# Performance work log

Hardware: AMD Instinct MI355X
Metric: run time of the kernel (lower is better)

The kernel has to match this reference:

```python
import jax, jax.numpy as jnp
import numpy as np

EPS = 1e-5
LOCAL_WINDOW = 256
NUM_HEADS = 16


def _layernorm(x, g, b):
    m = jnp.mean(x, axis=-1, keepdims=True)
    v = jnp.mean(jnp.square(x - m), axis=-1, keepdims=True)
    return (x - m) * jax.lax.rsqrt(v + EPS) * g + b


def _rotate_half(x):
    x1, x2 = jnp.split(x, 2, axis=-1)
    return jnp.concatenate([-x2, x1], axis=-1)


def _rope_cos_sin(s, d, base=10000.0):
    half = d // 2
    inv_freq = 1.0 / base ** (jnp.arange(half, dtype=jnp.float32) / float(half))
    t = jnp.arange(s, dtype=jnp.float32)
    freqs = jnp.einsum('s,d->sd', t, inv_freq)          # [s, half]
    emb = jnp.concatenate([freqs, freqs], axis=-1)       # [s, d]
    return jnp.cos(emb)[None, None, :, :], jnp.sin(emb)[None, None, :, :]


def setup_inputs() -> dict:
    key = jax.random.key(0)
    ks = jax.random.split(key, 8)
    B, S, D, F = 2, 2048, 1024, 4096
    sc = lambda d: 1.0 / np.sqrt(d)
    return {
        'x': jax.random.normal(ks[0], (B, S, D), jnp.float32),
        'w_qkv': jax.random.normal(ks[1], (D, 3 * D), jnp.float32) * sc(D),
        'w_out': jax.random.normal(ks[2], (D, D), jnp.float32) * sc(D),
        'g1': jnp.ones((D,), jnp.float32),
        'b1': jnp.zeros((D,), jnp.float32),
        'g2': jnp.ones((D,), jnp.float32),
        'b2': jnp.zeros((D,), jnp.float32),
        'w_gate': jax.random.normal(ks[3], (D, F), jnp.float32) * sc(D),
        'b_gate': jnp.zeros((F,), jnp.float32),
        'w_up': jax.random.normal(ks[4], (D, F), jnp.float32) * sc(D),
        'b_up': jnp.zeros((F,), jnp.float32),
        'w_down': jax.random.normal(ks[5], (F, D), jnp.float32) * sc(F),
        'b_down': jnp.zeros((D,), jnp.float32),
    }


def reference(x, w_qkv, w_out, g1, b1, g2, b2, w_gate, b_gate, w_up, b_up, w_down, b_down):
    B, S, D = x.shape
    H = NUM_HEADS
    hd = D // H

    # ---- pre-norm + RoPE self-attention ----
    y = _layernorm(x, g1, b1)
    qkv = jnp.einsum('bsd,de->bse', y, w_qkv)
    q, k, v = jnp.split(qkv, 3, axis=-1)
    split_heads = lambda t: t.reshape(B, S, H, hd).transpose(0, 2, 1, 3)  # [b,h,s,hd]
    q, k, v = split_heads(q), split_heads(k), split_heads(v)

    cos, sin = _rope_cos_sin(S, hd)
    q = q * cos + _rotate_half(q) * sin
    k = k * cos + _rotate_half(k) * sin

    scale = float(hd) ** -0.5
    logits = jnp.einsum('bhid,bhjd->bhij', q, k) * scale

    i = jnp.arange(S)[:, None]
    j = jnp.arange(S)[None, :]
    can = (jnp.abs(j - i) <= LOCAL_WINDOW) & (j <= i)    # local + causal band
    logits = jnp.where(can[None, None], logits, jnp.float32(-1e9))

    attn = jax.nn.softmax(logits, axis=-1)
    o = jnp.einsum('bhij,bhjd->bhid', attn, v)
    o = o.transpose(0, 2, 1, 3).reshape(B, S, D)
    x = x + jnp.einsum('bsd,de->bse', o, w_out)

    # ---- pre-norm + SwiGLU MLP ----
    y = _layernorm(x, g2, b2)
    gate = jnp.einsum('bsd,df->bsf', y, w_gate) + b_gate
    up = jnp.einsum('bsd,df->bsf', y, w_up) + b_up
    gated = gate * jax.nn.silu(up)
    x = x + jnp.einsum('bsf,fd->bsd', gated, w_down) + b_down
    return x
```

## Files before the change

kernel.cpp:

```cpp
#include <hip/hip_runtime.h>

typedef unsigned short u16;
typedef unsigned long long u64;
typedef __attribute__((ext_vector_type(8))) short bf16x8;
typedef __attribute__((ext_vector_type(4))) float f32x4;

__device__ inline u16 f2bf(float f) {
  unsigned int u = __float_as_uint(f);
  u += 0x7fffu + ((u >> 16) & 1u);
  return (u16)(u >> 16);
}
__device__ inline float bf2f(u16 h) { return __uint_as_float(((unsigned int)h) << 16); }

__device__ inline void gload_lds16(const void* gp, void* lp) {
  __builtin_amdgcn_global_load_lds(
      (const __attribute__((address_space(1))) unsigned int*)gp,
      (__attribute__((address_space(3))) unsigned int*)lp, 16, 0, 0);
}

__global__ __launch_bounds__(256) void ln_kernel(const float* __restrict__ x,
                                                 const float* __restrict__ g,
                                                 const float* __restrict__ beta,
                                                 u16* __restrict__ y) {
  __shared__ float red[8];
  const int row = blockIdx.x;
  const int t = threadIdx.x;
  const float4 xv = *(const float4*)(x + (long)row * 1024 + t * 4);
  float s = xv.x + xv.y + xv.z + xv.w;
  float sq = xv.x * xv.x + xv.y * xv.y + xv.z * xv.z + xv.w * xv.w;
#pragma unroll
  for (int d = 1; d < 64; d <<= 1) {
    s += __shfl_xor(s, d);
    sq += __shfl_xor(sq, d);
  }
  if ((t & 63) == 0) { red[t >> 6] = s; red[4 + (t >> 6)] = sq; }
  __syncthreads();
  s = red[0] + red[1] + red[2] + red[3];
  sq = red[4] + red[5] + red[6] + red[7];
  const float mean = s * (1.f / 1024.f);
  const float var = sq * (1.f / 1024.f) - mean * mean;
  const float inv = rsqrtf(var + 1e-5f);
  float xe[4] = {xv.x, xv.y, xv.z, xv.w};
  u16 ov[4];
#pragma unroll
  for (int e = 0; e < 4; ++e)
    ov[e] = f2bf((xe[e] - mean) * inv * g[t * 4 + e] + beta[t * 4 + e]);
  *(u64*)(y + (long)row * 1024 + t * 4) = *(u64*)ov;
}

__global__ __launch_bounds__(256) void transpose_bf16(const float* __restrict__ in,
                                                      u16* __restrict__ out,
                                                      int R, int C) {
  __shared__ float tile[64][33];
  const int t = threadIdx.x;
  const int tx = t & 31, ty = t >> 5;
  const int rx = t & 63, cy = t >> 6;
  const long r0 = (long)blockIdx.y * 64, c0 = (long)blockIdx.x * 32;
#pragma unroll
  for (int i = 0; i < 8; ++i)
    tile[ty + i * 8][tx] = in[(r0 + ty + i * 8) * C + c0 + tx];
  __syncthreads();
#pragma unroll
  for (int i = 0; i < 8; ++i)
    out[(c0 + i * 4 + cy) * R + r0 + rx] = f2bf(tile[rx][i * 4 + cy]);
}

__global__ __launch_bounds__(256) void trig_kernel(float* __restrict__ tbl) {
  const int i = blockIdx.x * 256 + threadIdx.x;
  const int s = i >> 5, d0 = i & 31;
  const float inv = exp2f((float)d0 * (-13.287712379549449f / 32.f));
  float sn, cs;
  sincosf((float)s * inv, &sn, &cs);
  tbl[i] = cs;
  tbl[65536 + i] = sn;
}

__global__ __launch_bounds__(64, 4) void attn_kernel(const u16* __restrict__ qr,
                                                     const u16* __restrict__ kr,
                                                     const u16* __restrict__ vt,
                                                     u16* __restrict__ o) {
  __shared__ __attribute__((aligned(16))) u16 Pl[16][40];
  int wg = blockIdx.x;
  wg = (wg & 7) * 512 + (wg >> 3);
  const int qt = wg & 127;
  const int bh = wg >> 7;
  const int qs = qt * 16;
  const int l = threadIdx.x;
  const int lr = l & 15, lg = l >> 4;
  const long bho = (long)(bh >> 4) * 2048 * 1024 + (long)(bh & 15) * 64;
  const long vtb = (long)bh * 64 * 2048;

  const u16* qp = qr + bho + (long)(qs + lr) * 1024 + lg * 8;
  const bf16x8 aq0 = *(const bf16x8*)qp;
  const bf16x8 aq1 = *(const bf16x8*)(qp + 32);

  f32x4 oacc[4];
#pragma unroll
  for (int nt = 0; nt < 4; ++nt) { oacc[nt][0] = 0.f; oacc[nt][1] = 0.f; oacc[nt][2] = 0.f; oacc[nt][3] = 0.f; }
  float m_[4], ls[4];
#pragma unroll
  for (int r = 0; r < 4; ++r) { m_[r] = -1e30f; ls[r] = 0.f; }

  for (int ch = 0; ch < 9; ++ch) {
    const int j0 = qs - 256 + ch * 32;
    if (j0 + 32 <= 0) continue;

    const int jc0u = j0 + lr;
    const int jc1u = j0 + 16 + lr;
    const int jc0 = min(max(jc0u, 0), 2047);
    const int jc1 = min(max(jc1u, 0), 2047);
    const u16* kp0 = kr + bho + (long)jc0 * 1024 + lg * 8;
    const u16* kp1 = kr + bho + (long)jc1 * 1024 + lg * 8;
    const bf16x8 b00 = *(const bf16x8*)kp0;
    const bf16x8 b01 = *(const bf16x8*)(kp0 + 32);
    const bf16x8 b10 = *(const bf16x8*)kp1;
    const bf16x8 b11 = *(const bf16x8*)(kp1 + 32);

    f32x4 z; z[0] = 0.f; z[1] = 0.f; z[2] = 0.f; z[3] = 0.f;
    f32x4 s0 = __builtin_amdgcn_mfma_f32_16x16x32_bf16(aq0, b00, z, 0, 0, 0);
    s0 = __builtin_amdgcn_mfma_f32_16x16x32_bf16(aq1, b01, s0, 0, 0, 0);
    f32x4 s1 = __builtin_amdgcn_mfma_f32_16x16x32_bf16(aq0, b10, z, 0, 0, 0);
    s1 = __builtin_amdgcn_mfma_f32_16x16x32_bf16(aq1, b11, s1, 0, 0, 0);

    float p0[4], p1[4], al[4];
#pragma unroll
    for (int r = 0; r < 4; ++r) {
      const int qg = qs + lg * 4 + r;
      const bool v0 = (jc0u >= 0) & (jc0u <= qg) & (qg - jc0u <= 256);
      const bool v1 = (jc1u >= 0) & (jc1u <= qg) & (qg - jc1u <= 256);
      const float t0 = v0 ? s0[r] : -1e30f;
      const float t1 = v1 ? s1[r] : -1e30f;
      float mx = fmaxf(t0, t1);
      mx = fmaxf(mx, __shfl_xor(mx, 1));
      mx = fmaxf(mx, __shfl_xor(mx, 2));
      mx = fmaxf(mx, __shfl_xor(mx, 4));
      mx = fmaxf(mx, __shfl_xor(mx, 8));
      const float mn = fmaxf(m_[r], mx);
      if (mn < -1e29f) {
        al[r] = 1.f; p0[r] = 0.f; p1[r] = 0.f;
      } else {
        al[r] = __expf(m_[r] - mn);
        p0[r] = (t0 < -1e29f) ? 0.f : __expf(t0 - mn);
        p1[r] = (t1 < -1e29f) ? 0.f : __expf(t1 - mn);
      }
      m_[r] = mn;
      float rs = p0[r] + p1[r];
      rs += __shfl_xor(rs, 1);
      rs += __shfl_xor(rs, 2);
      rs += __shfl_xor(rs, 4);
      rs += __shfl_xor(rs, 8);
      ls[r] = ls[r] * al[r] + rs;
    }
#pragma unroll
    for (int r = 0; r < 4; ++r) {
      Pl[lg * 4 + r][lr] = f2bf(p0[r]);
      Pl[lg * 4 + r][lr + 16] = f2bf(p1[r]);
    }
    asm volatile("s_waitcnt lgkmcnt(0)" ::: "memory");
    const bf16x8 pa = *(const bf16x8*)(&Pl[lr][lg * 8]);

    const int jb = min(max(j0 + lg * 8, 0), 2040);
    const u16* vp = vt + vtb + (long)lr * 2048 + jb;
#pragma unroll
    for (int nt = 0; nt < 4; ++nt) {
      const bf16x8 bv = *(const bf16x8*)(vp + (long)(nt * 16) * 2048);
      f32x4 oa = oacc[nt];
#pragma unroll
      for (int r = 0; r < 4; ++r) oa[r] *= al[r];
      oacc[nt] = __builtin_amdgcn_mfma_f32_16x16x32_bf16(pa, bv, oa, 0, 0, 0);
    }
  }
#pragma unroll
  for (int nt = 0; nt < 4; ++nt)
#pragma unroll
    for (int r = 0; r < 4; ++r) {
      const long qg = qs + lg * 4 + r;
      o[bho + qg * 1024 + nt * 16 + lr] = f2bf(oacc[nt][r] / ls[r]);
    }
}

__device__ __forceinline__ void stage_half(u16* lds, int ldsbase,
                                           const u16* gp, int ld, int col,
                                           int tid, int w) {
  const int r0 = tid >> 3;
  const int sw = ((tid & 7) ^ (r0 & 7)) << 3;
  gload_lds16(gp + (long)r0 * ld + col + sw, lds + ldsbase + w * 512);
  gload_lds16(gp + (long)(r0 + 64) * ld + col + sw, lds + ldsbase + 4096 + w * 512);
}

template <int EPI>
__global__ __launch_bounds__(512, 2) void gemm8p(const u16* __restrict__ A,
                                                 const u16* __restrict__ BT,
                                                 u16* __restrict__ Cb,
                                                 const float* __restrict__ bias,
                                                 const u16* __restrict__ gate,
                                                 float* __restrict__ Cf0,
                                                 float* __restrict__ Cf1,
                                                 u16* __restrict__ P1,
                                                 u16* __restrict__ P2,
                                                 const float* __restrict__ tbl,
                                                 int M, int N, int Kfull, int Kl) {
  __shared__ __attribute__((aligned(16))) u16 lds[81920];
  const int tid = threadIdx.x;
  const int w = tid >> 6, l = tid & 63;
  const int lr = l & 15, lg = l >> 4;
  const int l7 = l & 7;
  const int wr = w >> 2, wc = w & 3;
  const int nbx = N >> 8, nby = M >> 8;
  int wg = blockIdx.x;
  { const int cpx = gridDim.x >> 3; wg = (wg & 7) * cpx + (wg >> 3); }
  const int z = wg / (nbx * nby);
  const int rem = wg % (nbx * nby);
  const long m0 = (long)(rem / nbx) * 256;
  const long n0 = (long)(rem % nbx) * 256;
  const long koff = (long)z * Kl;
  const int NT = Kl >> 6;

  f32x4 acc[8][4];
#pragma unroll
  for (int i = 0; i < 8; ++i)
#pragma unroll
    for (int j = 0; j < 4; ++j) { acc[i][j][0] = 0.f; acc[i][j][1] = 0.f; acc[i][j][2] = 0.f; acc[i][j][3] = 0.f; }

  const u16* Alo = A + m0 * Kfull + koff;
  const u16* Ahi = A + (m0 + 128) * Kfull + koff;
  const u16* Blo = BT + n0 * Kfull + koff;
  const u16* Bhi = BT + (n0 + 128) * Kfull + koff;

  stage_half(lds, 0, Alo, Kfull, 0, tid, w);
  stage_half(lds, 8192, Ahi, Kfull, 0, tid, w);
  stage_half(lds, 49152, Blo, Kfull, 0, tid, w);
  stage_half(lds, 57344, Bhi, Kfull, 0, tid, w);
  stage_half(lds, 16384, Alo, Kfull, 64, tid, w);
  stage_half(lds, 24576, Ahi, Kfull, 64, tid, w);
  stage_half(lds, 65536, Blo, Kfull, 64, tid, w);
  stage_half(lds, 73728, Bhi, Kfull, 64, tid, w);
  asm volatile("s_waitcnt vmcnt(8)" ::: "memory");
  __builtin_amdgcn_s_barrier();

  for (int t = 0; t < NT; ++t) {
    const int abuf = t % 3;
    int sA = abuf + 2; if (sA >= 3) sA -= 3;
    const int p = t & 1;
    const int baA = abuf * 16384 + wr * 8192;
    const int bB = 49152 + p * 16384;
    bf16x8 b[4][2];
#pragma unroll
    for (int q = 0; q < 4; ++q) {
      bf16x8 a[2][2];
#pragma unroll
      for (int m2 = 0; m2 < 2; ++m2) {
        const int rowA = (q * 2 + m2) * 16 + lr;
#pragma unroll
        for (int kh = 0; kh < 2; ++kh)
          a[m2][kh] = *(const bf16x8*)(lds + baA + rowA * 64 + (((kh * 4 + lg) ^ l7) << 3));
      }
      if (q == 0) {
#pragma unroll
        for (int fn = 0; fn < 4; ++fn) {
          const int rb = wc * 64 + fn * 16 + lr;
#pragma unroll
          for (int kh = 0; kh < 2; ++kh)
            b[fn][kh] = *(const bf16x8*)(lds + bB + (rb >> 7) * 8192 + (rb & 127) * 64 + (((kh * 4 + lg) ^ l7) << 3));
        }
      }
      if (t + 2 < NT) {
        if (q == 0) stage_half(lds, sA * 16384, Alo, Kfull, (t + 2) * 64, tid, w);
        if (q == 1) stage_half(lds, sA * 16384 + 8192, Ahi, Kfull, (t + 2) * 64, tid, w);
        if (q == 2) stage_half(lds, bB, Blo, Kfull, (t + 2) * 64, tid, w);
        if (q == 3) stage_half(lds, bB + 8192, Bhi, Kfull, (t + 2) * 64, tid, w);
      }

      __builtin_amdgcn_s_barrier();
      asm volatile("s_waitcnt lgkmcnt(0)" ::: "memory");
      __builtin_amdgcn_s_setprio(1);
#pragma unroll
      for (int m2 = 0; m2 < 2; ++m2)
#pragma unroll
        for (int fn = 0; fn < 4; ++fn)
#pragma unroll
          for (int kh = 0; kh < 2; ++kh)
            acc[q * 2 + m2][fn] = __builtin_amdgcn_mfma_f32_16x16x32_bf16(a[m2][kh], b[fn][kh], acc[q * 2 + m2][fn], 0, 0, 0);
      __builtin_amdgcn_s_setprio(0);
      if (q == 3) {
        if (t + 2 < NT) { asm volatile("s_waitcnt vmcnt(8)" ::: "memory"); }
        else            { asm volatile("s_waitcnt vmcnt(0)" ::: "memory"); }
      }
      __builtin_amdgcn_s_barrier();
    }
  }

  if constexpr (EPI == 6) {
    const int regn = (int)((n0 + wc * 64) >> 10);
    if (regn < 2) {
      const float scale = (regn == 0) ? 0.125f : 1.f;
      u16* dst = (regn == 0) ? Cb : P1;
      const int cbase = (int)(n0 & 1023) + wc * 64 + lr;
#pragma unroll
      for (int fm = 0; fm < 8; ++fm) {
        const long mr = m0 + wr * 128 + fm * 16 + lg * 4;
#pragma unroll
        for (int fn = 0; fn < 2; ++fn) {
          const int c1 = cbase + fn * 16;
          const int d0 = fn * 16 + lr;
#pragma unroll
          for (int r = 0; r < 4; ++r) {
            const long row = mr + r;
            const int s = (int)(row & 2047);
            const float cs = tbl[(s << 5) + d0];
            const float sn = tbl[65536 + (s << 5) + d0];
            const float x1v = acc[fm][fn][r], x2v = acc[fm][fn + 2][r];
            dst[row * 1024 + c1] = f2bf((x1v * cs - x2v * sn) * scale);
            dst[row * 1024 + c1 + 32] = f2bf((x2v * cs + x1v * sn) * scale);
          }
        }
      }
    } else {
#pragma unroll
      for (int fm = 0; fm < 8; ++fm) {
        const long mr = m0 + wr * 128 + fm * 16 + lg * 4;
        const int bb = (int)(mr >> 11);
        const int s = (int)(mr & 2047);
#pragma unroll
        for (int fn = 0; fn < 4; ++fn) {
          const int ncv = (int)(n0 - 2048) + wc * 64 + fn * 16 + lr;
          const int h = ncv >> 6, d = ncv & 63;
          u16 pk[4];
#pragma unroll
          for (int r = 0; r < 4; ++r) pk[r] = f2bf(acc[fm][fn][r]);
          *(u64*)(P2 + (long)(bb * 16 + h) * 131072 + (long)d * 2048 + s) = *(u64*)pk;
        }
      }
    }
    return;
  }

  float* Cf = nullptr;
  if constexpr (EPI == 0) Cf = (z < 2 ? Cf0 : Cf1) + (long)(z & 1) * M * N;

#pragma unroll
  for (int fm = 0; fm < 8; ++fm) {
    const long mr = m0 + wr * 128 + fm * 16 + lg * 4;
#pragma unroll
    for (int fn = 0; fn < 4; ++fn) {
      const long nc = n0 + wc * 64 + fn * 16 + lr;
#pragma unroll
      for (int r = 0; r < 4; ++r) {
        const long idx = (mr + r) * N + nc;
        const float v = acc[fm][fn][r];
        if constexpr (EPI == 5) {
          Cb[idx] = f2bf(v);
        } else if constexpr (EPI == 2) {
          Cb[idx] = f2bf(v + bias[nc]);
        } else if constexpr (EPI == 3) {
          const float u = v + bias[nc];
          const float sg = 1.f / (1.f + __expf(-u));
          Cb[idx] = f2bf(bf2f(gate[idx]) * u * sg);
        } else if constexpr (EPI == 0) {
          Cf[idx] = v;
        }
      }
    }
  }
}

__global__ __launch_bounds__(256) void combine_ln(const float* __restrict__ p0,
                                                  const float* __restrict__ p1,
                                                  const float* __restrict__ x,
                                                  const float* __restrict__ g,
                                                  const float* __restrict__ beta,
                                                  float* __restrict__ x1,
                                                  u16* __restrict__ y) {
  __shared__ float red[8];
  const long MN = (long)4096 * 1024;
  const int row = blockIdx.x;
  const int t = threadIdx.x;
  const long base = (long)row * 1024 + t * 4;
  const float4 a = *(const float4*)(p0 + base);
  const float4 b = *(const float4*)(p0 + MN + base);
  const float4 c = *(const float4*)(p1 + base);
  const float4 d = *(const float4*)(p1 + MN + base);
  const float4 r = *(const float4*)(x + base);
  float v[4] = {a.x + b.x + c.x + d.x + r.x, a.y + b.y + c.y + d.y + r.y,
                a.z + b.z + c.z + d.z + r.z, a.w + b.w + c.w + d.w + r.w};
  *(float4*)(x1 + base) = *(float4*)v;
  float s = v[0] + v[1] + v[2] + v[3];
  float sq = v[0] * v[0] + v[1] * v[1] + v[2] * v[2] + v[3] * v[3];
#pragma unroll
  for (int dd = 1; dd < 64; dd <<= 1) {
    s += __shfl_xor(s, dd);
    sq += __shfl_xor(sq, dd);
  }
  if ((t & 63) == 0) { red[t >> 6] = s; red[4 + (t >> 6)] = sq; }
  __syncthreads();
  s = red[0] + red[1] + red[2] + red[3];
  sq = red[4] + red[5] + red[6] + red[7];
  const float mean = s * (1.f / 1024.f);
  const float var = sq * (1.f / 1024.f) - mean * mean;
  const float inv = rsqrtf(var + 1e-5f);
  u16 ov[4];
#pragma unroll
  for (int e = 0; e < 4; ++e)
    ov[e] = f2bf((v[e] - mean) * inv * g[t * 4 + e] + beta[t * 4 + e]);
  *(u64*)(y + base) = *(u64*)ov;
}

__global__ __launch_bounds__(256) void combine4(const float* __restrict__ p0,
                                                const float* __restrict__ p1,
                                                const float* __restrict__ res,
                                                const float* __restrict__ bias,
                                                float* __restrict__ out) {
  const long MN = (long)4096 * 1024;
  const long i = ((long)blockIdx.x * 256 + threadIdx.x) * 4;
  const float4 a = *(const float4*)(p0 + i);
  const float4 b = *(const float4*)(p0 + MN + i);
  const float4 c = *(const float4*)(p1 + i);
  const float4 d = *(const float4*)(p1 + MN + i);
  const float4 r = *(const float4*)(res + i);
  const float4 bb = *(const float4*)(bias + (int)(i & 1023));
  float4 o;
  o.x = a.x + b.x + c.x + d.x + r.x + bb.x;
  o.y = a.y + b.y + c.y + d.y + r.y + bb.y;
  o.z = a.z + b.z + c.z + d.z + r.z + bb.z;
  o.w = a.w + b.w + c.w + d.w + r.w + bb.w;
  *(float4*)(out + i) = o;
}

extern "C" void kernel_launch(void* const* d_in, const int* in_sizes, int n_in,
                              void* d_out, int out_size, void* d_ws, size_t ws_size,
                              hipStream_t stream) {
  (void)in_sizes; (void)n_in; (void)out_size; (void)ws_size;
  const float* x      = (const float*)d_in[0];
  const float* w_qkv  = (const float*)d_in[1];
  const float* w_out  = (const float*)d_in[2];
  const float* g1     = (const float*)d_in[3];
  const float* b1     = (const float*)d_in[4];
  const float* g2     = (const float*)d_in[5];
  const float* b2     = (const float*)d_in[6];
  const float* w_gate = (const float*)d_in[7];
  const float* b_gate = (const float*)d_in[8];
  const float* w_up   = (const float*)d_in[9];
  const float* b_up   = (const float*)d_in[10];
  const float* w_down = (const float*)d_in[11];
  const float* b_down = (const float*)d_in[12];
  float* out = (float*)d_out;

  const size_t MB = 1u << 20;
  char* ws = (char*)d_ws;
  u16*   wdownT = (u16*)(ws + 0 * MB);
  u16*   y      = (u16*)(ws + 8 * MB);
  u16*   wqkvT  = (u16*)(ws + 16 * MB);
  u16*   woutT  = (u16*)(ws + 22 * MB);
  u16*   wgateT = (u16*)(ws + 24 * MB);
  u16*   wupT   = (u16*)(ws + 32 * MB);
  u16*   qr_    = (u16*)(ws + 40 * MB);
  u16*   kr_    = (u16*)(ws + 48 * MB);
  u16*   vt     = (u16*)(ws + 56 * MB);
  float* trig   = (float*)(ws + 64 * MB);
  u16*   o_     = (u16*)(ws + 64 * MB);
  float* part0  = (float*)(ws + 72 * MB);
  float* part1  = (float*)(ws + 104 * MB);
  float* x1     = (float*)(ws + 56 * MB);
  u16*   gbuf   = (u16*)(ws + 72 * MB);
  u16*   gated  = (u16*)(ws + 104 * MB);
  float* pd0    = (float*)(ws + 16 * MB);
  float* pd1    = (float*)(ws + 72 * MB);

  const dim3 blk(256);
  transpose_bf16<<<dim3(3072 / 32, 1024 / 64), blk, 0, stream>>>(w_qkv, wqkvT, 1024, 3072);
  transpose_bf16<<<dim3(1024 / 32, 1024 / 64), blk, 0, stream>>>(w_out, woutT, 1024, 1024);
  transpose_bf16<<<dim3(4096 / 32, 1024 / 64), blk, 0, stream>>>(w_gate, wgateT, 1024, 4096);
  transpose_bf16<<<dim3(4096 / 32, 1024 / 64), blk, 0, stream>>>(w_up, wupT, 1024, 4096);
  transpose_bf16<<<dim3(1024 / 32, 4096 / 64), blk, 0, stream>>>(w_down, wdownT, 4096, 1024);
  trig_kernel<<<256, blk, 0, stream>>>(trig);

  ln_kernel<<<4096, blk, 0, stream>>>(x, g1, b1, y);
  gemm8p<6><<<dim3((3072 / 256) * (4096 / 256)), dim3(512), 0, stream>>>(
      y, wqkvT, qr_, nullptr, nullptr, nullptr, nullptr, kr_, vt, trig,
      4096, 3072, 1024, 1024);
  attn_kernel<<<4096, dim3(64), 0, stream>>>(qr_, kr_, vt, o_);
  gemm8p<0><<<dim3(4 * 16 * 4), dim3(512), 0, stream>>>(
      o_, woutT, nullptr, nullptr, nullptr, part0, part1, nullptr, nullptr, nullptr,
      4096, 1024, 1024, 256);
  combine_ln<<<4096, blk, 0, stream>>>(part0, part1, x, g2, b2, x1, y);
  gemm8p<2><<<dim3((4096 / 256) * (4096 / 256)), dim3(512), 0, stream>>>(
      y, wgateT, gbuf, b_gate, nullptr, nullptr, nullptr, nullptr, nullptr, nullptr,
      4096, 4096, 1024, 1024);
  gemm8p<3><<<dim3((4096 / 256) * (4096 / 256)), dim3(512), 0, stream>>>(
      y, wupT, gated, b_up, gbuf, nullptr, nullptr, nullptr, nullptr, nullptr,
      4096, 4096, 1024, 1024);
  gemm8p<0><<<dim3(4 * 16 * 4), dim3(512), 0, stream>>>(
      gated, wdownT, nullptr, nullptr, nullptr, pd0, pd1, nullptr, nullptr, nullptr,
      4096, 1024, 4096, 1024);
  combine4<<<4096, blk, 0, stream>>>(pd0, pd1, x1, b_down, out);
}
```

Measured before the change: 283.8 us.

## Fuse gate and up projections into one GEMM with interleaved weights

Gate and up weights are transposed into a single interleaved B matrix, 16 columns of gate followed by 16 of up, so one N=8192 GEMM produces both. A new epilogue pairs the adjacent gate/up fragments in registers and applies bias plus SiLU gating directly. This removes the intermediate bf16 gate buffer write and its re-read, and one kernel launch. The up bias is passed through the tbl pointer, and the epilogue layout depends on wc*64 tiles aligning with the 32-column interleave.

After: 277.9 us. -2.1%, faster.

```diff
diff --git a/kernel.cpp b/kernel.cpp
--- a/kernel.cpp
+++ b/kernel.cpp
@@ -63,6 +63,26 @@
 #pragma unroll
   for (int i = 0; i < 8; ++i)
     out[(c0 + i * 4 + cy) * R + r0 + rx] = f2bf(tile[rx][i * 4 + cy]);
+}
+
+__global__ __launch_bounds__(256) void transpose_ilv(const float* __restrict__ in,
+                                                     u16* __restrict__ out,
+                                                     int R, int C, int off) {
+  __shared__ float tile[64][33];
+  const int t = threadIdx.x;
+  const int tx = t & 31, ty = t >> 5;
+  const int rx = t & 63, cy = t >> 6;
+  const long r0 = (long)blockIdx.y * 64, c0 = (long)blockIdx.x * 32;
+#pragma unroll
+  for (int i = 0; i < 8; ++i)
+    tile[ty + i * 8][tx] = in[(r0 + ty + i * 8) * C + c0 + tx];
+  __syncthreads();
+#pragma unroll
+  for (int i = 0; i < 8; ++i) {
+    const int c = (int)c0 + i * 4 + cy;
+    const long v = ((long)(c >> 4) << 5) + off + (c & 15);
+    out[v * R + r0 + rx] = f2bf(tile[rx][i * 4 + cy]);
+  }
 }
 
 __global__ __launch_bounds__(256) void trig_kernel(float* __restrict__ tbl) {
@@ -193,7 +213,6 @@
                                                  const u16* __restrict__ BT,
                                                  u16* __restrict__ Cb,
                                                  const float* __restrict__ bias,
-                                                 const u16* __restrict__ gate,
                                                  float* __restrict__ Cf0,
                                                  float* __restrict__ Cf1,
                                                  u16* __restrict__ P1,
@@ -335,9 +354,29 @@
     return;
   }
 
-  float* Cf = nullptr;
-  if constexpr (EPI == 0) Cf = (z < 2 ? Cf0 : Cf1) + (long)(z & 1) * M * N;
-
+  if constexpr (EPI == 7) {
+    const int rcb = (int)((n0 + wc * 64) >> 1);
+#pragma unroll
+    for (int fm = 0; fm < 8; ++fm) {
+      const long mr = m0 + wr * 128 + fm * 16 + lg * 4;
+#pragma unroll
+      for (int fp = 0; fp < 2; ++fp) {
+        const int rc = rcb + fp * 16 + lr;
+        const float bg = bias[rc];
+        const float bu = tbl[rc];
+#pragma unroll
+        for (int r = 0; r < 4; ++r) {
+          const float g = acc[fm][2 * fp][r] + bg;
+          const float u = acc[fm][2 * fp + 1][r] + bu;
+          const float sg = 1.f / (1.f + __expf(-u));
+          Cb[(mr + r) * 4096 + rc] = f2bf(g * u * sg);
+        }
+      }
+    }
+    return;
+  }
+
+  float* Cf = (z < 2 ? Cf0 : Cf1) + (long)(z & 1) * M * N;
 #pragma unroll
   for (int fm = 0; fm < 8; ++fm) {
     const long mr = m0 + wr * 128 + fm * 16 + lg * 4;
@@ -345,21 +384,8 @@
     for (int fn = 0; fn < 4; ++fn) {
       const long nc = n0 + wc * 64 + fn * 16 + lr;
 #pragma unroll
-      for (int r = 0; r < 4; ++r) {
-        const long idx = (mr + r) * N + nc;
-        const float v = acc[fm][fn][r];
-        if constexpr (EPI == 5) {
-          Cb[idx] = f2bf(v);
-        } else if constexpr (EPI == 2) {
-          Cb[idx] = f2bf(v + bias[nc]);
-        } else if constexpr (EPI == 3) {
-          const float u = v + bias[nc];
-          const float sg = 1.f / (1.f + __expf(-u));
-          Cb[idx] = f2bf(bf2f(gate[idx]) * u * sg);
-        } else if constexpr (EPI == 0) {
-          Cf[idx] = v;
-        }
-      }
+      for (int r = 0; r < 4; ++r)
+        Cf[(mr + r) * N + nc] = acc[fm][fn][r];
     }
   }
 }
@@ -451,8 +477,7 @@
   u16*   y      = (u16*)(ws + 8 * MB);
   u16*   wqkvT  = (u16*)(ws + 16 * MB);
   u16*   woutT  = (u16*)(ws + 22 * MB);
-  u16*   wgateT = (u16*)(ws + 24 * MB);
-  u16*   wupT   = (u16*)(ws + 32 * MB);
+  u16*   wguT   = (u16*)(ws + 24 * MB);
   u16*   qr_    = (u16*)(ws + 40 * MB);
   u16*   kr_    = (u16*)(ws + 48 * MB);
   u16*   vt     = (u16*)(ws + 56 * MB);
@@ -461,7 +486,6 @@
   float* part0  = (float*)(ws + 72 * MB);
   float* part1  = (float*)(ws + 104 * MB);
   float* x1     = (float*)(ws + 56 * MB);
-  u16*   gbuf   = (u16*)(ws + 72 * MB);
   u16*   gated  = (u16*)(ws + 104 * MB);
   float* pd0    = (float*)(ws + 16 * MB);
   float* pd1    = (float*)(ws + 72 * MB);
@@ -469,28 +493,25 @@
   const dim3 blk(256);
   transpose_bf16<<<dim3(3072 / 32, 1024 / 64), blk, 0, stream>>>(w_qkv, wqkvT, 1024, 3072);
   transpose_bf16<<<dim3(1024 / 32, 1024 / 64), blk, 0, stream>>>(w_out, woutT, 1024, 1024);
-  transpose_bf16<<<dim3(4096 / 32, 1024 / 64), blk, 0, stream>>>(w_gate, wgateT, 1024, 4096);
-  transpose_bf16<<<dim3(4096 / 32, 1024 / 64), blk, 0, stream>>>(w_up, wupT, 1024, 4096);
+  transpose_ilv<<<dim3(4096 / 32, 1024 / 64), blk, 0, stream>>>(w_gate, wguT, 1024, 4096, 0);
+  transpose_ilv<<<dim3(4096 / 32, 1024 / 64), blk, 0, stream>>>(w_up, wguT, 1024, 4096, 16);
   transpose_bf16<<<dim3(1024 / 32, 4096 / 64), blk, 0, stream>>>(w_down, wdownT, 4096, 1024);
   trig_kernel<<<256, blk, 0, stream>>>(trig);
 
   ln_kernel<<<4096, blk, 0, stream>>>(x, g1, b1, y);
   gemm8p<6><<<dim3((3072 / 256) * (4096 / 256)), dim3(512), 0, stream>>>(
-      y, wqkvT, qr_, nullptr, nullptr, nullptr, nullptr, kr_, vt, trig,
+      y, wqkvT, qr_, nullptr, nullptr, nullptr, kr_, vt, trig,
       4096, 3072, 1024, 1024);
   attn_kernel<<<4096, dim3(64), 0, stream>>>(qr_, kr_, vt, o_);
   gemm8p<0><<<dim3(4 * 16 * 4), dim3(512), 0, stream>>>(
-      o_, woutT, nullptr, nullptr, nullptr, part0, part1, nullptr, nullptr, nullptr,
+      o_, woutT, nullptr, nullptr, part0, part1, nullptr, nullptr, nullptr,
       4096, 1024, 1024, 256);
   combine_ln<<<4096, blk, 0, stream>>>(part0, part1, x, g2, b2, x1, y);
-  gemm8p<2><<<dim3((4096 / 256) * (4096 / 256)), dim3(512), 0, stream>>>(
-      y, wgateT, gbuf, b_gate, nullptr, nullptr, nullptr, nullptr, nullptr, nullptr,
-      4096, 4096, 1024, 1024);
-  gemm8p<3><<<dim3((4096 / 256) * (4096 / 256)), dim3(512), 0, stream>>>(
-      y, wupT, gated, b_up, gbuf, nullptr, nullptr, nullptr, nullptr, nullptr,
-      4096, 4096, 1024, 1024);
+  gemm8p<7><<<dim3((8192 / 256) * (4096 / 256)), dim3(512), 0, stream>>>(
+      y, wguT, gated, b_gate, nullptr, nullptr, nullptr, nullptr, b_up,
+      4096, 8192, 1024, 1024);
   gemm8p<0><<<dim3(4 * 16 * 4), dim3(512), 0, stream>>>(
-      gated, wdownT, nullptr, nullptr, nullptr, pd0, pd1, nullptr, nullptr, nullptr,
+      gated, wdownT, nullptr, nullptr, pd0, pd1, nullptr, nullptr, nullptr,
       4096, 1024, 4096, 1024);
   combine4<<<4096, blk, 0, stream>>>(pd0, pd1, x1, b_down, out);
 }
```
